# Performance work log

Hardware: AMD Instinct MI355X
Metric: run time of the kernel (lower is better)

The kernel has to match this reference:

```python
import jax, jax.numpy as jnp
import numpy as np

B, N, D = 4, 1024, 1024      # batch, seq_len, query_dim
H, DH = 16, 64               # heads, dim_head; inner = H*DH = 1024
INNER = H * DH
SCALE = DH ** -0.5


def setup_inputs() -> dict:
    key = jax.random.key(0)
    ks = jax.random.split(key, 8)
    x = jax.random.normal(ks[0], (B, N, D), dtype=jnp.float32)
    rel_pos = jax.random.normal(ks[1], (B * H, N, N), dtype=jnp.float32)
    query_mask = jax.random.randint(ks[2], (B, N), 0, 2).astype(bool)
    context_mask = jax.random.randint(ks[3], (B, N), 0, 2).astype(bool)
    # Linear weights stored (in, out); to_q/to_kv have no bias, to_out has bias.
    Wq = jax.random.normal(ks[4], (D, INNER), dtype=jnp.float32) / np.sqrt(D)
    Wkv = jax.random.normal(ks[5], (D, 2 * INNER), dtype=jnp.float32) / np.sqrt(D)
    Wo = jax.random.normal(ks[6], (INNER, D), dtype=jnp.float32) / np.sqrt(INNER)
    bo = jax.random.normal(ks[7], (D,), dtype=jnp.float32) * 0.01
    return {"x": x, "rel_pos": rel_pos, "query_mask": query_mask,
            "context_mask": context_mask, "Wq": Wq, "Wkv": Wkv, "Wo": Wo, "bo": bo}


def reference(x, rel_pos, query_mask, context_mask, Wq, Wkv, Wo, bo):
    # Self-attention (context = x)
    q = x @ Wq                                 # [B, N, INNER]
    kv = x @ Wkv                               # [B, N, 2*INNER]
    k, v = jnp.split(kv, 2, axis=-1)
    # (b n (h d)) -> (b h n d)
    split_heads = lambda t: t.reshape(B, N, H, DH).transpose(0, 2, 1, 3)
    q, k, v = map(split_heads, (q, k, v))
    sim = jnp.einsum('bhid,bhjd->bhij', q, k) * SCALE
    sim = sim + rel_pos.reshape(B, H, N, N)
    neg = -jnp.finfo(sim.dtype).max
    # query_mask: (b i) -> mask rows; context_mask: (b j) -> mask cols
    sim = jnp.where(query_mask[:, None, :, None], sim, neg)
    sim = jnp.where(context_mask[:, None, None, :], sim, neg)
    attn = jax.nn.softmax(sim, axis=-1)
    out = jnp.einsum('bhij,bhjd->bhid', attn, v)    # [B, H, N, DH]
    out = out.transpose(0, 2, 1, 3).reshape(B, N, INNER)
    return out @ Wo + bo
```

## Files before the change

kernel.cpp:

```cpp
#include <hip/hip_runtime.h>


#define NEGMAX 3.402823466e+38f

typedef short short8 __attribute__((ext_vector_type(8)));
typedef float f32x4 __attribute__((ext_vector_type(4)));

__device__ __forceinline__ unsigned short f2bf(float f) {
  unsigned int u = __float_as_uint(f);
  u += 0x7FFFu + ((u >> 16) & 1u);
  return (unsigned short)(u >> 16);
}

__device__ __forceinline__ void stage16(const void* g, void* lds_base, int lane) {
#if __has_builtin(__builtin_amdgcn_global_load_lds)
  __builtin_amdgcn_global_load_lds(
      (const __attribute__((address_space(1))) unsigned int*)g,
      (__attribute__((address_space(3))) unsigned int*)lds_base, 16, 0, 0);
#else
  *(int4*)((char*)lds_base + lane * 16) = *(const int4*)g;
#endif
}

__global__ void cast_x_k(const float* __restrict__ x, unsigned short* __restrict__ xb) {
  int i = (blockIdx.x * 256 + threadIdx.x) * 4;
  float4 v = *(const float4*)(x + i);
  ushort4 o;
  o.x = f2bf(v.x); o.y = f2bf(v.y); o.z = f2bf(v.z); o.w = f2bf(v.w);
  *(ushort4*)(xb + i) = o;
}

__global__ __launch_bounds__(256) void tcast_k(const float* __restrict__ src, int ldsrc,
                                               unsigned short* __restrict__ dst) {
  __shared__ float T[64][65];
  const int n0 = blockIdx.x * 64, d0 = blockIdx.y * 64;
  const int tx = threadIdx.x & 63, ty = threadIdx.x >> 6;
#pragma unroll
  for (int k = 0; k < 16; ++k) {
    int dl = k * 4 + ty;
    T[dl][tx] = src[(size_t)(d0 + dl) * ldsrc + n0 + tx];
  }
  __syncthreads();
#pragma unroll
  for (int k = 0; k < 16; ++k) {
    int nl = k * 4 + ty;
    dst[(size_t)(n0 + nl) * 1024 + d0 + tx] = f2bf(T[tx][nl]);
  }
}

__global__ __launch_bounds__(256) void gemm_bt_k(
    const unsigned short* __restrict__ A, const unsigned short* __restrict__ Bt,
    unsigned short* __restrict__ qws, unsigned short* __restrict__ kws,
    unsigned short* __restrict__ vtws) {
  constexpr int K = 1024;
  constexpr int NKB = K / 32;
  __shared__ alignas(16) unsigned short As[128 * 32];
  __shared__ alignas(16) unsigned short Bs[128 * 32];
  const int tid = threadIdx.x;
  const int lane = tid & 63, w = tid >> 6;
  const int quad = lane >> 4, lanelo = lane & 15;
  const int tRow = blockIdx.y * 128, tCol = blockIdx.x * 128;
  const int wr = (w >> 1) * 64, wc = (w & 1) * 64;
  const char* AgB = (const char*)(A + (size_t)tRow * K);
  const char* BgB = (const char*)(Bt + (size_t)tCol * K);
  const int c0 = tid, c1 = tid + 256;
  const size_t a0off = (size_t)(c0 >> 2) * 2048 + (c0 & 3) * 16;
  const size_t a1off = (size_t)(c1 >> 2) * 2048 + (c1 & 3) * 16;
  char* ldsA0 = (char*)As + w * 1024;
  char* ldsA1 = (char*)As + 4096 + w * 1024;
  char* ldsB0 = (char*)Bs + w * 1024;
  char* ldsB1 = (char*)Bs + 4096 + w * 1024;

  f32x4 acc[4][4];
#pragma unroll
  for (int i = 0; i < 4; ++i)
#pragma unroll
    for (int j = 0; j < 4; ++j) acc[i][j] = (f32x4){0.f, 0.f, 0.f, 0.f};

  for (int kb = 0; kb < NKB; ++kb) {
    if (kb) __syncthreads();
    const size_t ko = (size_t)kb * 64;
    stage16(AgB + a0off + ko, ldsA0, lane);
    stage16(AgB + a1off + ko, ldsA1, lane);
    stage16(BgB + a0off + ko, ldsB0, lane);
    stage16(BgB + a1off + ko, ldsB1, lane);
    __syncthreads();

    short8 af[4], bf[4];
#pragma unroll
    for (int i = 0; i < 4; ++i)
      af[i] = *(const short8*)(As + (wr + i * 16 + lanelo) * 32 + quad * 8);
#pragma unroll
    for (int j = 0; j < 4; ++j)
      bf[j] = *(const short8*)(Bs + (wc + j * 16 + lanelo) * 32 + quad * 8);
#pragma unroll
    for (int i = 0; i < 4; ++i)
#pragma unroll
      for (int j = 0; j < 4; ++j)
        acc[i][j] = __builtin_amdgcn_mfma_f32_16x16x32_bf16(af[i], bf[j], acc[i][j], 0, 0, 0);
  }

#pragma unroll
  for (int i = 0; i < 4; ++i) {
    int row = tRow + wr + i * 16 + quad * 4;
    int b_ = row >> 10;
    int npos = row & 1023;
#pragma unroll
    for (int j = 0; j < 4; ++j) {
      int col = tCol + wc + j * 16 + lanelo;
      if (col < 2048) {
        unsigned short* dst = (col < 1024) ? qws : kws;
        int c = col & 1023;
        int hh = c >> 6, dh = c & 63;
        size_t base = ((size_t)(b_ * 16 + hh) * 1024 + npos) * 64 + dh;
#pragma unroll
        for (int r = 0; r < 4; ++r) dst[base + (size_t)r * 64] = f2bf(acc[i][j][r]);
      } else {
        int c = col - 2048;
        ushort4 pk;
        pk.x = f2bf(acc[i][j][0]);
        pk.y = f2bf(acc[i][j][1]);
        pk.z = f2bf(acc[i][j][2]);
        pk.w = f2bf(acc[i][j][3]);
        *(ushort4*)&vtws[((size_t)(b_ * 16 + (c >> 6)) * 64 + (c & 63)) * 1024 + npos] = pk;
      }
    }
  }
}

__global__ __launch_bounds__(256) void gemm64_k(
    const unsigned short* __restrict__ A, const unsigned short* __restrict__ Bt,
    const float* __restrict__ bias, float* __restrict__ Cout) {
  constexpr int K = 1024;
  constexpr int NKB = K / 32;
  __shared__ alignas(16) unsigned short As[64 * 32];
  __shared__ alignas(16) unsigned short Bs[64 * 32];
  const int tid = threadIdx.x;
  const int lane = tid & 63, w = tid >> 6;
  const int quad = lane >> 4, lanelo = lane & 15;
  const int tRow = blockIdx.y * 64, tCol = blockIdx.x * 64;
  const char* AgB = (const char*)(A + (size_t)tRow * K);
  const char* BgB = (const char*)(Bt + (size_t)tCol * K);
  const size_t aoff = (size_t)(tid >> 2) * 2048 + (tid & 3) * 16;
  char* ldsA = (char*)As + w * 1024;
  char* ldsB = (char*)Bs + w * 1024;

  f32x4 acc[4];
#pragma unroll
  for (int j = 0; j < 4; ++j) acc[j] = (f32x4){0.f, 0.f, 0.f, 0.f};

  for (int kb = 0; kb < NKB; ++kb) {
    if (kb) __syncthreads();
    const size_t ko = (size_t)kb * 64;
    stage16(AgB + aoff + ko, ldsA, lane);
    stage16(BgB + aoff + ko, ldsB, lane);
    __syncthreads();

    short8 af = *(const short8*)(As + (w * 16 + lanelo) * 32 + quad * 8);
#pragma unroll
    for (int j = 0; j < 4; ++j) {
      short8 bf = *(const short8*)(Bs + (j * 16 + lanelo) * 32 + quad * 8);
      acc[j] = __builtin_amdgcn_mfma_f32_16x16x32_bf16(af, bf, acc[j], 0, 0, 0);
    }
  }

  const int row = tRow + w * 16 + quad * 4;
#pragma unroll
  for (int j = 0; j < 4; ++j) {
    int col = tCol + j * 16 + lanelo;
    float bv = bias[col];
#pragma unroll
    for (int r = 0; r < 4; ++r)
      Cout[(size_t)(row + r) * 1024 + col] = acc[j][r] + bv;
  }
}

__global__ __launch_bounds__(256)
__attribute__((amdgpu_waves_per_eu(4, 4)))
void attn_k(
    const unsigned short* __restrict__ q_ws, const unsigned short* __restrict__ k_ws,
    const unsigned short* __restrict__ vt_ws, const float* __restrict__ rel,
    const int* __restrict__ qmask, const int* __restrict__ cmask,
    unsigned short* __restrict__ aout) {
  constexpr float SCALE = 0.125f;
  __shared__ alignas(16) unsigned short Kl[2 * 64 * 64];
  __shared__ alignas(16) unsigned short Pl[4 * 16 * 72];
  __shared__ float rbias[1024];

  const int tid = threadIdx.x;
  const int w = tid >> 6, lane = tid & 63;
  const int quad = lane >> 4, lanelo = lane & 15;

  const int flat = blockIdx.y * 16 + blockIdx.x;
  const int virt = (flat & 7) * 128 + (flat >> 3);
  const int bh = virt >> 4, qblk = virt & 15;
  const int b_ = bh >> 4, h = bh & 15;
  const int qrow0 = qblk * 64 + w * 16;

  const unsigned short* kg = k_ws + (size_t)bh * 65536;
  const unsigned short* vg = vt_ws + (size_t)bh * 65536;
  const float* relg = rel + ((size_t)bh * 1024 + qrow0) * 1024;
  unsigned short* pw = Pl + w * 16 * 72;

  const int srow = lane >> 3;
  const int spx = (((lane & 7) ^ srow) << 4);
#define STAGE_K(buf, key0n)                                                     \
  {                                                                             \
    _Pragma("unroll")                                                           \
    for (int i_ = 0; i_ < 2; ++i_) {                                            \
      int row_ = w * 16 + i_ * 8 + srow;                                        \
      stage16((const char*)kg + (size_t)((key0n) + row_) * 128 + spx,           \
              (char*)Kl + (buf) * 8192 + w * 2048 + i_ * 1024, lane);           \
    }                                                                           \
  }

  STAGE_K(0, 0);

  for (int i = tid; i < 1024; i += 256)
    rbias[i] = (cmask[b_ * 1024 + i] != 0) ? 0.f : -NEGMAX;

  const unsigned short* qg = q_ws + ((size_t)bh * 1024 + qrow0) * 64;
  short8 qf0 = *(const short8*)(qg + (size_t)lanelo * 64 + quad * 8);
  short8 qf1 = *(const short8*)(qg + (size_t)lanelo * 64 + 32 + quad * 8);

  const bool qok = qmask[b_ * 1024 + qrow0 + lanelo] != 0;

  f32x4 o[4];
#pragma unroll
  for (int g = 0; g < 4; ++g) o[g] = (f32x4){0.f, 0.f, 0.f, 0.f};
  float m_run = -NEGMAX, l_run = 0.f;

  f32x4 rl[4];
#pragma unroll
  for (int c = 0; c < 4; ++c)
    rl[c] = *(const f32x4*)(relg + (size_t)lanelo * 1024 + c * 16 + quad * 4);

  const int sb = lanelo & 7;

  for (int kb = 0; kb < 16; ++kb) {
    const int key0 = kb * 64;
    const int cur = kb & 1;

    __syncthreads();
    if (kb + 1 < 16) STAGE_K(cur ^ 1, key0 + 64);

    short8 vf[8];
#pragma unroll
    for (int c2 = 0; c2 < 2; ++c2)
#pragma unroll
      for (int g = 0; g < 4; ++g)
        vf[c2 * 4 + g] = *(const short8*)(vg + (size_t)(g * 16 + lanelo) * 1024 +
                                          key0 + c2 * 32 + quad * 8);

    f32x4 s[4];
#pragma unroll
    for (int c = 0; c < 4; ++c) {
      const char* kbase = (const char*)Kl + cur * 8192 + (c * 16 + lanelo) * 128;
      short8 kfa = *(const short8*)(kbase + ((quad ^ sb) << 4));
      short8 kfb = *(const short8*)(kbase + (((4 + quad) ^ sb) << 4));
      s[c] = (f32x4){0.f, 0.f, 0.f, 0.f};
      s[c] = __builtin_amdgcn_mfma_f32_16x16x32_bf16(kfa, qf0, s[c], 0, 0, 0);
      s[c] = __builtin_amdgcn_mfma_f32_16x16x32_bf16(kfb, qf1, s[c], 0, 0, 0);
    }

    f32x4 rln[4];
    if (kb + 1 < 16) {
#pragma unroll
      for (int c = 0; c < 4; ++c)
        rln[c] = *(const f32x4*)(relg + (size_t)lanelo * 1024 + key0 + 64 + c * 16 + quad * 4);
    }

    float mloc = -NEGMAX;
#pragma unroll
    for (int c = 0; c < 4; ++c) {
      f32x4 rb = *(const f32x4*)(rbias + key0 + c * 16 + quad * 4);
#pragma unroll
      for (int r = 0; r < 4; ++r) {
        float v = s[c][r] * SCALE + rl[c][r] + rb[r];
        v = qok ? v : -NEGMAX;
        s[c][r] = v;
        mloc = fmaxf(mloc, v);
      }
    }
    mloc = fmaxf(mloc, __shfl_xor(mloc, 16));
    mloc = fmaxf(mloc, __shfl_xor(mloc, 32));

    if (!__all(mloc - m_run <= 8.f)) {
      float mnew = fmaxf(m_run, mloc);
      float alpha = __expf(m_run - mnew);
      m_run = mnew;
      l_run *= alpha;
      float a4[4];
#pragma unroll
      for (int r = 0; r < 4; ++r) a4[r] = __shfl(alpha, quad * 4 + r, 16);
#pragma unroll
      for (int g = 0; g < 4; ++g)
#pragma unroll
        for (int r = 0; r < 4; ++r) o[g][r] *= a4[r];
    }

    float ps = 0.f;
#pragma unroll
    for (int c = 0; c < 4; ++c) {
      ushort4 pk;
      float p0 = __expf(s[c][0] - m_run);
      float p1 = __expf(s[c][1] - m_run);
      float p2 = __expf(s[c][2] - m_run);
      float p3 = __expf(s[c][3] - m_run);
      ps += (p0 + p1) + (p2 + p3);
      pk.x = f2bf(p0); pk.y = f2bf(p1); pk.z = f2bf(p2); pk.w = f2bf(p3);
      *(ushort4*)((char*)pw + lanelo * 144 + c * 32 + quad * 8) = pk;
    }
    ps += __shfl_xor(ps, 16);
    ps += __shfl_xor(ps, 32);
    l_run += ps;

#pragma unroll
    for (int c2 = 0; c2 < 2; ++c2) {
      short8 pa = *(const short8*)((const char*)pw + lanelo * 144 + c2 * 64 + quad * 16);
#pragma unroll
      for (int g = 0; g < 4; ++g)
        o[g] = __builtin_amdgcn_mfma_f32_16x16x32_bf16(pa, vf[c2 * 4 + g], o[g], 0, 0, 0);
    }

    if (kb + 1 < 16) {
#pragma unroll
      for (int c = 0; c < 4; ++c) rl[c] = rln[c];
    }
  }
#undef STAGE_K

  float invl = 1.f / l_run;
#pragma unroll
  for (int r = 0; r < 4; ++r) {
    float iv = __shfl(invl, quad * 4 + r, 16);
    size_t row = (size_t)(b_ * 1024 + qrow0 + quad * 4 + r) * 1024;
#pragma unroll
    for (int g = 0; g < 4; ++g)
      aout[row + h * 64 + g * 16 + lanelo] = f2bf(o[g][r] * iv);
  }
}

extern "C" void kernel_launch(void* const* d_in, const int* in_sizes, int n_in,
                              void* d_out, int out_size, void* d_ws, size_t ws_size,
                              hipStream_t stream) {
  const float* x = (const float*)d_in[0];
  const float* rel = (const float*)d_in[1];
  const int* qmask = (const int*)d_in[2];
  const int* cmask = (const int*)d_in[3];
  const float* Wq = (const float*)d_in[4];
  const float* Wkv = (const float*)d_in[5];
  const float* Wo = (const float*)d_in[6];
  const float* bo = (const float*)d_in[7];
  float* out = (float*)d_out;

  char* ws = (char*)d_ws;
  const size_t MB = 1024 * 1024;
  unsigned short* w3t = (unsigned short*)(ws);
  unsigned short* wot = (unsigned short*)(ws + 6 * MB);
  unsigned short* xb  = (unsigned short*)(ws + 8 * MB);
  unsigned short* qws = (unsigned short*)(ws + 16 * MB);
  unsigned short* kws = (unsigned short*)(ws + 24 * MB);
  unsigned short* vtws = (unsigned short*)(ws + 32 * MB);
  unsigned short* aout = xb;

  cast_x_k<<<4096, 256, 0, stream>>>(x, xb);
  tcast_k<<<dim3(16, 16), 256, 0, stream>>>(Wq, 1024, w3t);
  tcast_k<<<dim3(32, 16), 256, 0, stream>>>(Wkv, 2048, w3t + (size_t)1024 * 1024);
  tcast_k<<<dim3(16, 16), 256, 0, stream>>>(Wo, 1024, wot);
  gemm_bt_k<<<dim3(24, 32), 256, 0, stream>>>(xb, w3t, qws, kws, vtws);
  attn_k<<<dim3(16, 64), 256, 0, stream>>>(qws, kws, vtws, rel, qmask, cmask, aout);
  gemm64_k<<<dim3(16, 64), 256, 0, stream>>>(aout, wot, bo, out);
}
```

Measured before the change: 495.9 us.

## Split attention into single-wave blocks loading K directly into registers

The attention kernel now launches one 64-thread wave per block, each handling 16 query rows, with four times as many blocks. K tiles are loaded straight from global memory into registers with a one-step prefetch instead of being staged through double-buffered LDS behind __syncthreads. The context-mask bias is read per tile from global memory rather than from a precomputed LDS array. This removes block-level barriers and LDS staging, at the cost of each wave reloading K and the mask independently and carrying more register pressure.

```diff
diff --git a/kernel.cpp b/kernel.cpp
--- a/kernel.cpp
+++ b/kernel.cpp
@@ -175,7 +175,7 @@
   }
 }
 
-__global__ __launch_bounds__(256)
+__global__ __launch_bounds__(64)
 __attribute__((amdgpu_waves_per_eu(4, 4)))
 void attn_k(
     const unsigned short* __restrict__ q_ws, const unsigned short* __restrict__ k_ws,
@@ -183,41 +183,21 @@
     const int* __restrict__ qmask, const int* __restrict__ cmask,
     unsigned short* __restrict__ aout) {
   constexpr float SCALE = 0.125f;
-  __shared__ alignas(16) unsigned short Kl[2 * 64 * 64];
-  __shared__ alignas(16) unsigned short Pl[4 * 16 * 72];
-  __shared__ float rbias[1024];
-
-  const int tid = threadIdx.x;
-  const int w = tid >> 6, lane = tid & 63;
+  __shared__ alignas(16) unsigned short Pl[16 * 72];
+
+  const int lane = threadIdx.x;
   const int quad = lane >> 4, lanelo = lane & 15;
 
-  const int flat = blockIdx.y * 16 + blockIdx.x;
-  const int virt = (flat & 7) * 128 + (flat >> 3);
-  const int bh = virt >> 4, qblk = virt & 15;
+  const int flat = blockIdx.y * 64 + blockIdx.x;
+  const int virt = (flat & 7) * 512 + (flat >> 3);
+  const int bh = virt >> 6, qblk = virt & 63;
   const int b_ = bh >> 4, h = bh & 15;
-  const int qrow0 = qblk * 64 + w * 16;
+  const int qrow0 = qblk * 16;
 
   const unsigned short* kg = k_ws + (size_t)bh * 65536;
   const unsigned short* vg = vt_ws + (size_t)bh * 65536;
   const float* relg = rel + ((size_t)bh * 1024 + qrow0) * 1024;
-  unsigned short* pw = Pl + w * 16 * 72;
-
-  const int srow = lane >> 3;
-  const int spx = (((lane & 7) ^ srow) << 4);
-#define STAGE_K(buf, key0n)                                                     \
-  {                                                                             \
-    _Pragma("unroll")                                                           \
-    for (int i_ = 0; i_ < 2; ++i_) {                                            \
-      int row_ = w * 16 + i_ * 8 + srow;                                        \
-      stage16((const char*)kg + (size_t)((key0n) + row_) * 128 + spx,           \
-              (char*)Kl + (buf) * 8192 + w * 2048 + i_ * 1024, lane);           \
-    }                                                                           \
-  }
-
-  STAGE_K(0, 0);
-
-  for (int i = tid; i < 1024; i += 256)
-    rbias[i] = (cmask[b_ * 1024 + i] != 0) ? 0.f : -NEGMAX;
+  const int* cmg = cmask + b_ * 1024;
 
   const unsigned short* qg = q_ws + ((size_t)bh * 1024 + qrow0) * 64;
   short8 qf0 = *(const short8*)(qg + (size_t)lanelo * 64 + quad * 8);
@@ -230,19 +210,30 @@
   for (int g = 0; g < 4; ++g) o[g] = (f32x4){0.f, 0.f, 0.f, 0.f};
   float m_run = -NEGMAX, l_run = 0.f;
 
+  short8 kf[8];
+#pragma unroll
+  for (int c = 0; c < 4; ++c) {
+    const unsigned short* krow = kg + (size_t)(c * 16 + lanelo) * 64;
+    kf[2 * c]     = *(const short8*)(krow + quad * 8);
+    kf[2 * c + 1] = *(const short8*)(krow + 32 + quad * 8);
+  }
   f32x4 rl[4];
 #pragma unroll
   for (int c = 0; c < 4; ++c)
     rl[c] = *(const f32x4*)(relg + (size_t)lanelo * 1024 + c * 16 + quad * 4);
 
-  const int sb = lanelo & 7;
-
   for (int kb = 0; kb < 16; ++kb) {
     const int key0 = kb * 64;
-    const int cur = kb & 1;
-
-    __syncthreads();
-    if (kb + 1 < 16) STAGE_K(cur ^ 1, key0 + 64);
+
+    short8 kfn[8];
+    if (kb + 1 < 16) {
+#pragma unroll
+      for (int c = 0; c < 4; ++c) {
+        const unsigned short* krow = kg + (size_t)(key0 + 64 + c * 16 + lanelo) * 64;
+        kfn[2 * c]     = *(const short8*)(krow + quad * 8);
+        kfn[2 * c + 1] = *(const short8*)(krow + 32 + quad * 8);
+      }
+    }
 
     short8 vf[8];
 #pragma unroll
@@ -251,16 +242,17 @@
       for (int g = 0; g < 4; ++g)
         vf[c2 * 4 + g] = *(const short8*)(vg + (size_t)(g * 16 + lanelo) * 1024 +
                                           key0 + c2 * 32 + quad * 8);
+    int4 cm4[4];
+#pragma unroll
+    for (int c = 0; c < 4; ++c)
+      cm4[c] = *(const int4*)(cmg + key0 + c * 16 + quad * 4);
 
     f32x4 s[4];
 #pragma unroll
     for (int c = 0; c < 4; ++c) {
-      const char* kbase = (const char*)Kl + cur * 8192 + (c * 16 + lanelo) * 128;
-      short8 kfa = *(const short8*)(kbase + ((quad ^ sb) << 4));
-      short8 kfb = *(const short8*)(kbase + (((4 + quad) ^ sb) << 4));
       s[c] = (f32x4){0.f, 0.f, 0.f, 0.f};
-      s[c] = __builtin_amdgcn_mfma_f32_16x16x32_bf16(kfa, qf0, s[c], 0, 0, 0);
-      s[c] = __builtin_amdgcn_mfma_f32_16x16x32_bf16(kfb, qf1, s[c], 0, 0, 0);
+      s[c] = __builtin_amdgcn_mfma_f32_16x16x32_bf16(kf[2 * c], qf0, s[c], 0, 0, 0);
+      s[c] = __builtin_amdgcn_mfma_f32_16x16x32_bf16(kf[2 * c + 1], qf1, s[c], 0, 0, 0);
     }
 
     f32x4 rln[4];
@@ -273,14 +265,20 @@
     float mloc = -NEGMAX;
 #pragma unroll
     for (int c = 0; c < 4; ++c) {
-      f32x4 rb = *(const f32x4*)(rbias + key0 + c * 16 + quad * 4);
-#pragma unroll
-      for (int r = 0; r < 4; ++r) {
-        float v = s[c][r] * SCALE + rl[c][r] + rb[r];
-        v = qok ? v : -NEGMAX;
-        s[c][r] = v;
-        mloc = fmaxf(mloc, v);
-      }
+      float rb0 = (cm4[c].x != 0) ? 0.f : -NEGMAX;
+      float rb1 = (cm4[c].y != 0) ? 0.f : -NEGMAX;
+      float rb2 = (cm4[c].z != 0) ? 0.f : -NEGMAX;
+      float rb3 = (cm4[c].w != 0) ? 0.f : -NEGMAX;
+      float v0 = s[c][0] * SCALE + rl[c][0] + rb0;
+      float v1 = s[c][1] * SCALE + rl[c][1] + rb1;
+      float v2 = s[c][2] * SCALE + rl[c][2] + rb2;
+      float v3 = s[c][3] * SCALE + rl[c][3] + rb3;
+      v0 = qok ? v0 : -NEGMAX;
+      v1 = qok ? v1 : -NEGMAX;
+      v2 = qok ? v2 : -NEGMAX;
+      v3 = qok ? v3 : -NEGMAX;
+      s[c][0] = v0; s[c][1] = v1; s[c][2] = v2; s[c][3] = v3;
+      mloc = fmaxf(mloc, fmaxf(fmaxf(v0, v1), fmaxf(v2, v3)));
     }
     mloc = fmaxf(mloc, __shfl_xor(mloc, 16));
     mloc = fmaxf(mloc, __shfl_xor(mloc, 32));
@@ -309,7 +307,7 @@
       float p3 = __expf(s[c][3] - m_run);
       ps += (p0 + p1) + (p2 + p3);
       pk.x = f2bf(p0); pk.y = f2bf(p1); pk.z = f2bf(p2); pk.w = f2bf(p3);
-      *(ushort4*)((char*)pw + lanelo * 144 + c * 32 + quad * 8) = pk;
+      *(ushort4*)((char*)Pl + lanelo * 144 + c * 32 + quad * 8) = pk;
     }
     ps += __shfl_xor(ps, 16);
     ps += __shfl_xor(ps, 32);
@@ -317,7 +315,7 @@
 
 #pragma unroll
     for (int c2 = 0; c2 < 2; ++c2) {
-      short8 pa = *(const short8*)((const char*)pw + lanelo * 144 + c2 * 64 + quad * 16);
+      short8 pa = *(const short8*)((const char*)Pl + lanelo * 144 + c2 * 64 + quad * 16);
 #pragma unroll
       for (int g = 0; g < 4; ++g)
         o[g] = __builtin_amdgcn_mfma_f32_16x16x32_bf16(pa, vf[c2 * 4 + g], o[g], 0, 0, 0);
@@ -326,9 +324,10 @@
     if (kb + 1 < 16) {
 #pragma unroll
       for (int c = 0; c < 4; ++c) rl[c] = rln[c];
-    }
-  }
-#undef STAGE_K
+#pragma unroll
+      for (int i = 0; i < 8; ++i) kf[i] = kfn[i];
+    }
+  }
 
   float invl = 1.f / l_run;
 #pragma unroll
@@ -369,6 +368,6 @@
   tcast_k<<<dim3(32, 16), 256, 0, stream>>>(Wkv, 2048, w3t + (size_t)1024 * 1024);
   tcast_k<<<dim3(16, 16), 256, 0, stream>>>(Wo, 1024, wot);
   gemm_bt_k<<<dim3(24, 32), 256, 0, stream>>>(xb, w3t, qws, kws, vtws);
-  attn_k<<<dim3(16, 64), 256, 0, stream>>>(qws, kws, vtws, rel, qmask, cmask, aout);
+  attn_k<<<dim3(64, 64), 64, 0, stream>>>(qws, kws, vtws, rel, qmask, cmask, aout);
   gemm64_k<<<dim3(16, 64), 256, 0, stream>>>(aout, wot, bo, out);
 }
```

After: 541.5 us. +9.2%, slower.

## Stage K, V and rel_pos tiles through double-buffered LDS with 32-key blocks

Applied to the files above, without the earlier changes.

The attention kernel now uses 32-key blocks instead of 64-key blocks. Each step asynchronously loads K, transposed V and the rel_pos bias tile into double-buffered LDS via global_load_lds, where before V and rel_pos were read directly from global memory into registers. This moves the dominant rel_pos stream and the V loads into the async pipeline, cuts register pressure, and drops the fixed waves_per_eu attribute. In exchange it doubles the number of iterations and barriers and uses more LDS per block, which may limit occupancy.

```diff
diff --git a/kernel.cpp b/kernel.cpp
--- a/kernel.cpp
+++ b/kernel.cpp
@@ -175,16 +175,16 @@
   }
 }
 
-__global__ __launch_bounds__(256)
-__attribute__((amdgpu_waves_per_eu(4, 4)))
-void attn_k(
+__global__ __launch_bounds__(256) void attn_k(
     const unsigned short* __restrict__ q_ws, const unsigned short* __restrict__ k_ws,
     const unsigned short* __restrict__ vt_ws, const float* __restrict__ rel,
     const int* __restrict__ qmask, const int* __restrict__ cmask,
     unsigned short* __restrict__ aout) {
   constexpr float SCALE = 0.125f;
-  __shared__ alignas(16) unsigned short Kl[2 * 64 * 64];
-  __shared__ alignas(16) unsigned short Pl[4 * 16 * 72];
+  __shared__ alignas(16) unsigned short Kl[2][2048];
+  __shared__ alignas(16) unsigned short Vl[2][4][512];
+  __shared__ alignas(16) float Rl[2][2048];
+  __shared__ alignas(16) unsigned short Pw[4][640];
   __shared__ float rbias[1024];
 
   const int tid = threadIdx.x;
@@ -199,22 +199,25 @@
 
   const unsigned short* kg = k_ws + (size_t)bh * 65536;
   const unsigned short* vg = vt_ws + (size_t)bh * 65536;
-  const float* relg = rel + ((size_t)bh * 1024 + qrow0) * 1024;
-  unsigned short* pw = Pl + w * 16 * 72;
-
-  const int srow = lane >> 3;
-  const int spx = (((lane & 7) ^ srow) << 4);
-#define STAGE_K(buf, key0n)                                                     \
+  const char* relg = (const char*)(rel + ((size_t)bh * 1024 + qblk * 64) * 1024);
+
+  const int l8 = lane & 7, l8h = lane >> 3;
+  const int sxk = ((l8 ^ l8h) << 4);
+
+#define STAGE(buf, k0)                                                          \
   {                                                                             \
-    _Pragma("unroll")                                                           \
-    for (int i_ = 0; i_ < 2; ++i_) {                                            \
-      int row_ = w * 16 + i_ * 8 + srow;                                        \
-      stage16((const char*)kg + (size_t)((key0n) + row_) * 128 + spx,           \
-              (char*)Kl + (buf) * 8192 + w * 2048 + i_ * 1024, lane);           \
-    }                                                                           \
-  }
-
-  STAGE_K(0, 0);
+    stage16((const char*)kg + (size_t)((k0) + w * 8 + l8h) * 128 + sxk,         \
+            (char*)&Kl[buf][0] + w * 1024, lane);                               \
+    stage16((const char*)vg + (size_t)(w * 16 + (lane & 15)) * 2048 +           \
+                (k0) * 2 + (lane >> 4) * 16,                                    \
+            (char*)&Vl[buf][w][0], lane);                                       \
+    stage16(relg + (size_t)(w * 16 + l8h) * 4096 + (k0) * 4 + sxk,              \
+            (char*)&Rl[buf][0] + w * 2048, lane);                               \
+    stage16(relg + (size_t)(w * 16 + 8 + l8h) * 4096 + (k0) * 4 + sxk,          \
+            (char*)&Rl[buf][0] + w * 2048 + 1024, lane);                        \
+  }
+
+  STAGE(0, 0);
 
   for (int i = tid; i < 1024; i += 256)
     rbias[i] = (cmask[b_ * 1024 + i] != 0) ? 0.f : -NEGMAX;
@@ -222,7 +225,6 @@
   const unsigned short* qg = q_ws + ((size_t)bh * 1024 + qrow0) * 64;
   short8 qf0 = *(const short8*)(qg + (size_t)lanelo * 64 + quad * 8);
   short8 qf1 = *(const short8*)(qg + (size_t)lanelo * 64 + 32 + quad * 8);
-
   const bool qok = qmask[b_ * 1024 + qrow0 + lanelo] != 0;
 
   f32x4 o[4];
@@ -230,57 +232,43 @@
   for (int g = 0; g < 4; ++g) o[g] = (f32x4){0.f, 0.f, 0.f, 0.f};
   float m_run = -NEGMAX, l_run = 0.f;
 
-  f32x4 rl[4];
-#pragma unroll
-  for (int c = 0; c < 4; ++c)
-    rl[c] = *(const f32x4*)(relg + (size_t)lanelo * 1024 + c * 16 + quad * 4);
-
   const int sb = lanelo & 7;
-
-  for (int kb = 0; kb < 16; ++kb) {
-    const int key0 = kb * 64;
+  char* pw = (char*)&Pw[w][0];
+
+  for (int kb = 0; kb < 32; ++kb) {
+    const int key0 = kb * 32;
     const int cur = kb & 1;
 
     __syncthreads();
-    if (kb + 1 < 16) STAGE_K(cur ^ 1, key0 + 64);
-
-    short8 vf[8];
-#pragma unroll
-    for (int c2 = 0; c2 < 2; ++c2)
-#pragma unroll
-      for (int g = 0; g < 4; ++g)
-        vf[c2 * 4 + g] = *(const short8*)(vg + (size_t)(g * 16 + lanelo) * 1024 +
-                                          key0 + c2 * 32 + quad * 8);
-
-    f32x4 s[4];
-#pragma unroll
-    for (int c = 0; c < 4; ++c) {
-      const char* kbase = (const char*)Kl + cur * 8192 + (c * 16 + lanelo) * 128;
-      short8 kfa = *(const short8*)(kbase + ((quad ^ sb) << 4));
-      short8 kfb = *(const short8*)(kbase + (((4 + quad) ^ sb) << 4));
+    if (kb + 1 < 32) STAGE(cur ^ 1, key0 + 32);
+
+    const char* Kb = (const char*)&Kl[cur][0];
+    f32x4 s[2];
+#pragma unroll
+    for (int c = 0; c < 2; ++c) {
+      const char* krow = Kb + (c * 16 + lanelo) * 128;
+      short8 kfa = *(const short8*)(krow + ((quad ^ sb) << 4));
+      short8 kfb = *(const short8*)(krow + (((4 + quad) ^ sb) << 4));
       s[c] = (f32x4){0.f, 0.f, 0.f, 0.f};
       s[c] = __builtin_amdgcn_mfma_f32_16x16x32_bf16(kfa, qf0, s[c], 0, 0, 0);
       s[c] = __builtin_amdgcn_mfma_f32_16x16x32_bf16(kfb, qf1, s[c], 0, 0, 0);
     }
 
-    f32x4 rln[4];
-    if (kb + 1 < 16) {
-#pragma unroll
-      for (int c = 0; c < 4; ++c)
-        rln[c] = *(const f32x4*)(relg + (size_t)lanelo * 1024 + key0 + 64 + c * 16 + quad * 4);
-    }
+    const char* Rb = (const char*)&Rl[cur][0] + (w * 16 + lanelo) * 128;
+    f32x4 rl0 = *(const f32x4*)(Rb + ((quad ^ sb) << 4));
+    f32x4 rl1 = *(const f32x4*)(Rb + (((4 + quad) ^ sb) << 4));
+    f32x4 rb0 = *(const f32x4*)(rbias + key0 + quad * 4);
+    f32x4 rb1 = *(const f32x4*)(rbias + key0 + 16 + quad * 4);
 
     float mloc = -NEGMAX;
 #pragma unroll
-    for (int c = 0; c < 4; ++c) {
-      f32x4 rb = *(const f32x4*)(rbias + key0 + c * 16 + quad * 4);
-#pragma unroll
-      for (int r = 0; r < 4; ++r) {
-        float v = s[c][r] * SCALE + rl[c][r] + rb[r];
-        v = qok ? v : -NEGMAX;
-        s[c][r] = v;
-        mloc = fmaxf(mloc, v);
-      }
+    for (int r = 0; r < 4; ++r) {
+      float v0 = s[0][r] * SCALE + rl0[r] + rb0[r];
+      float v1 = s[1][r] * SCALE + rl1[r] + rb1[r];
+      v0 = qok ? v0 : -NEGMAX;
+      v1 = qok ? v1 : -NEGMAX;
+      s[0][r] = v0; s[1][r] = v1;
+      mloc = fmaxf(mloc, fmaxf(v0, v1));
     }
     mloc = fmaxf(mloc, __shfl_xor(mloc, 16));
     mloc = fmaxf(mloc, __shfl_xor(mloc, 32));
@@ -301,7 +289,7 @@
 
     float ps = 0.f;
 #pragma unroll
-    for (int c = 0; c < 4; ++c) {
+    for (int c = 0; c < 2; ++c) {
       ushort4 pk;
       float p0 = __expf(s[c][0] - m_run);
       float p1 = __expf(s[c][1] - m_run);
@@ -309,26 +297,21 @@
       float p3 = __expf(s[c][3] - m_run);
       ps += (p0 + p1) + (p2 + p3);
       pk.x = f2bf(p0); pk.y = f2bf(p1); pk.z = f2bf(p2); pk.w = f2bf(p3);
-      *(ushort4*)((char*)pw + lanelo * 144 + c * 32 + quad * 8) = pk;
+      *(ushort4*)(pw + lanelo * 80 + c * 32 + quad * 8) = pk;
     }
     ps += __shfl_xor(ps, 16);
     ps += __shfl_xor(ps, 32);
     l_run += ps;
 
-#pragma unroll
-    for (int c2 = 0; c2 < 2; ++c2) {
-      short8 pa = *(const short8*)((const char*)pw + lanelo * 144 + c2 * 64 + quad * 16);
-#pragma unroll
-      for (int g = 0; g < 4; ++g)
-        o[g] = __builtin_amdgcn_mfma_f32_16x16x32_bf16(pa, vf[c2 * 4 + g], o[g], 0, 0, 0);
-    }
-
-    if (kb + 1 < 16) {
-#pragma unroll
-      for (int c = 0; c < 4; ++c) rl[c] = rln[c];
-    }
-  }
-#undef STAGE_K
+    short8 pa = *(const short8*)(pw + lanelo * 80 + quad * 16);
+    const char* Vb = (const char*)&Vl[cur][0][0];
+#pragma unroll
+    for (int g = 0; g < 4; ++g) {
+      short8 vb = *(const short8*)(Vb + g * 1024 + quad * 256 + lanelo * 16);
+      o[g] = __builtin_amdgcn_mfma_f32_16x16x32_bf16(pa, vb, o[g], 0, 0, 0);
+    }
+  }
+#undef STAGE
 
   float invl = 1.f / l_run;
 #pragma unroll
```

Measured after the change: 510.0 us. +2.8%, slower.
